# Optimization experiments

Measured on AMD Instinct MI355X. Metric: run time of the kernel, lower is better.

The kernel has to match this reference:

```python
import jax, jax.numpy as jnp
import numpy as np

E = 1024   # n_embd
H = 16     # n_heads
D = 64     # head_dim
G = 4      # n_kv_groups
F = 4096   # ffn hidden_dim
V = 32000  # vocab
L = 4      # n_layers (all full_attention)
B = 1
T = 2048
ROT = 16   # partial_rotary_factor 0.25 * head_dim 64, rounded to even
EPS = 1e-6
THETA = 10000.0


def rope_tables(seq_len):
    # matches compute_rope_params: inv_freq over even indices of rotary_dim
    inv_freq = 1.0 / (THETA ** (jnp.arange(0, ROT, 2, dtype=jnp.float32) / ROT))
    ang = jnp.arange(seq_len, dtype=jnp.float32)[:, None] * inv_freq[None, :]
    ang = jnp.concatenate([ang, ang], axis=1)  # [T, ROT]
    return jnp.cos(ang), jnp.sin(ang)


def rmsnorm(x, w):
    # torch RMSNorm: x * rsqrt(mean(x^2)+eps) * (1 + weight)
    xf = x.astype(jnp.float32)
    n = xf * jax.lax.rsqrt(jnp.mean(xf * xf, axis=-1, keepdims=True) + EPS)
    return (n * (1.0 + w)).astype(x.dtype)


def apply_rope(x, cos, sin):
    # x: [B, h, T, D]; cos/sin: [1, 1, T, ROT]; partial rotary on first ROT dims
    x_rot, x_pass = x[..., :ROT], x[..., ROT:]
    x1, x2 = x_rot[..., :ROT // 2], x_rot[..., ROT // 2:]
    rotated = jnp.concatenate([-x2, x1], axis=-1)
    return jnp.concatenate([x_rot * cos + rotated * sin, x_pass], axis=-1)


def _forward(tokens, emb, Wq, Wk, Wv, Wo, qn, kn, n1, n2, f1, f2, f3, fn, head):
    cos, sin = rope_tables(T)
    cos = cos[None, None]  # [1,1,T,ROT]
    sin = sin[None, None]
    mask = jnp.triu(jnp.ones((T, T), dtype=bool), k=1)  # True = masked
    scale = D ** -0.5
    x = emb[tokens]  # [B,T,E]

    def block(x, p):
        wq, wk, wv, wo, qw, kw, w1, w2, g1, g2, g3 = p
        h = rmsnorm(x, w1)
        # fused Q + gate projection -> [B,T,H,2D], chunk on last dim
        qg = (h @ wq).reshape(B, T, H, 2 * D)
        q = qg[..., :D].transpose(0, 2, 1, 3)            # [B,H,T,D]
        gate = qg[..., D:].reshape(B, T, H * D)          # [B,T,H*D]
        k = (h @ wk).reshape(B, T, G, D).transpose(0, 2, 1, 3)  # [B,G,T,D]
        v = (h @ wv).reshape(B, T, G, D).transpose(0, 2, 1, 3)
        q = rmsnorm(q, qw)
        k = rmsnorm(k, kw)
        q = apply_rope(q, cos, sin)
        k = apply_rope(k, cos, sin)
        k = jnp.repeat(k, H // G, axis=1)  # GQA expand -> [B,H,T,D]
        v = jnp.repeat(v, H // G, axis=1)
        scores = jnp.einsum('bhqd,bhkd->bhqk', q, k)
        scores = jnp.where(mask, -jnp.inf, scores) * scale
        w = jax.nn.softmax(scores.astype(jnp.float32), axis=-1).astype(q.dtype)
        ctx = jnp.einsum('bhqk,bhkd->bhqd', w, v)
        ctx = ctx.transpose(0, 2, 1, 3).reshape(B, T, H * D)
        ctx = ctx * jax.nn.sigmoid(gate)
        x = x + ctx @ wo
        h2 = rmsnorm(x, w2)
        ff = (jax.nn.silu(h2 @ g1) * (h2 @ g2)) @ g3
        return x + ff, None

    params = (Wq, Wk, Wv, Wo, qn, kn, n1, n2, f1, f2, f3)
    x, _ = jax.lax.scan(block, x, params)
    return rmsnorm(x, fn) @ head  # logits [B,T,V]


def setup_inputs() -> dict:
    key = jax.random.key(0)
    ks = jax.random.split(key, 16)
    s = 0.02
    rn = lambda k, shape, sc=s: jax.random.normal(k, shape, jnp.float32) * sc
    return {
        'tokens': jax.random.randint(ks[0], (B, T), 0, V),
        'emb': rn(ks[1], (V, E)),
        'Wq': rn(ks[2], (L, E, 2 * H * D)),
        'Wk': rn(ks[3], (L, E, G * D)),
        'Wv': rn(ks[4], (L, E, G * D)),
        'Wo': rn(ks[5], (L, H * D, E)),
        'qn': rn(ks[6], (L, D)),
        'kn': rn(ks[7], (L, D)),
        'n1': rn(ks[8], (L, E)),
        'n2': rn(ks[9], (L, E)),
        'f1': rn(ks[10], (L, E, F)),
        'f2': rn(ks[11], (L, E, F)),
        'f3': rn(ks[12], (L, F, E)),
        'fn': rn(ks[13], (E,)),
        'head': rn(ks[14], (E, V)),
    }


def reference(tokens, emb, Wq, Wk, Wv, Wo, qn, kn, n1, n2, f1, f2, f3, fn, head):
    return _forward(tokens, emb, Wq, Wk, Wv, Wo, qn, kn, n1, n2, f1, f2, f3, fn, head)
```

## Files before the change

kernel.cpp:

```cpp
#include <hip/hip_runtime.h>

#define T_LEN 2048
#define E_DIM 1024
#define H_N 16
#define G_N 4
#define D_H 64
#define F_DIM 4096
#define V_SZ 32000
#define L_N 4

typedef __attribute__((ext_vector_type(8))) __bf16 bf16x8;
typedef __attribute__((ext_vector_type(4))) float f32x4;

__device__ __forceinline__ unsigned short f2bf(float f){
  unsigned int u = __float_as_uint(f);
  unsigned int r = (u + 0x7FFFu + ((u >> 16) & 1u)) >> 16;
  return (unsigned short)r;
}

__device__ __forceinline__ f32x4 mfma16(bf16x8 a, bf16x8 b, f32x4 c){
  return __builtin_amdgcn_mfma_f32_16x16x32_bf16(a, b, c, 0, 0, 0);
}

__device__ __forceinline__ void gl16(const void* g, void* l){
  __builtin_amdgcn_global_load_lds((const __attribute__((address_space(1))) void*)g,
                                   (__attribute__((address_space(3))) void*)l, 16, 0, 0);
}

#define SBAR() __builtin_amdgcn_s_barrier()
#define LGK0() do{ asm volatile("s_waitcnt lgkmcnt(0)" ::: "memory"); __builtin_amdgcn_sched_barrier(0); }while(0)
#define VMC4() do{ asm volatile("s_waitcnt vmcnt(4)" ::: "memory"); __builtin_amdgcn_sched_barrier(0); }while(0)
#define VMC0() do{ asm volatile("s_waitcnt vmcnt(0)" ::: "memory"); __builtin_amdgcn_sched_barrier(0); }while(0)

#define QSCALE 0.1803368801111183f

__global__ __launch_bounds__(256) void embed_k(const float* __restrict__ emb,
                                               const int* __restrict__ tokens,
                                               float* __restrict__ x){
  int t = blockIdx.x;
  int tok = tokens[t];
  const float4* src = (const float4*)(emb + (size_t)tok * E_DIM);
  float4* dst = (float4*)(x + (size_t)t * E_DIM);
  dst[threadIdx.x] = src[threadIdx.x];
}

__global__ __launch_bounds__(256) void transpose_bf16(const float* __restrict__ src,
                                                      unsigned short* __restrict__ dst,
                                                      int R, int C){
  __shared__ float tile[32][33];
  int c0 = blockIdx.x * 32, r0 = blockIdx.y * 32;
  int tx = threadIdx.x & 31, ty = threadIdx.x >> 5;
  for (int i = 0; i < 4; i++){
    int r = ty + i * 8;
    tile[r][tx] = src[(size_t)(r0 + r) * C + c0 + tx];
  }
  __syncthreads();
  for (int i = 0; i < 4; i++){
    int r = ty + i * 8;
    dst[(size_t)(c0 + r) * R + r0 + tx] = f2bf(tile[tx][r]);
  }
}

__global__ __launch_bounds__(256) void rmsnorm_k(const float* __restrict__ x,
                                                 const float* __restrict__ w,
                                                 unsigned short* __restrict__ out){
  const int t = blockIdx.x, tid = threadIdx.x;
  const float4 v = ((const float4*)(x + (size_t)t * E_DIM))[tid];
  float ss = v.x*v.x + v.y*v.y + v.z*v.z + v.w*v.w;
  for (int m = 1; m < 64; m <<= 1) ss += __shfl_xor(ss, m);
  __shared__ float red[4];
  if ((tid & 63) == 0) red[tid >> 6] = ss;
  __syncthreads();
  ss = red[0] + red[1] + red[2] + red[3];
  const float r = rsqrtf(ss * (1.0f / E_DIM) + 1e-6f);
  const float4 wv = ((const float4*)w)[tid];
  ushort4 o;
  o.x = f2bf(v.x * r * (1.0f + wv.x));
  o.y = f2bf(v.y * r * (1.0f + wv.y));
  o.z = f2bf(v.z * r * (1.0f + wv.z));
  o.w = f2bf(v.w * r * (1.0f + wv.w));
  ((ushort4*)(out + (size_t)t * E_DIM))[tid] = o;
}

template<bool ADD>
__global__ __launch_bounds__(256) void gemm64_bt(const unsigned short* __restrict__ A,
                                                 const unsigned short* __restrict__ Bt,
                                                 float* __restrict__ C,
                                                 int M, int N, int K){
  __shared__ unsigned short As[64 * 32];
  __shared__ unsigned short Bs[128 * 32];
  const int tid = threadIdx.x;
  const int lane = tid & 63, w = tid >> 6;
  const int l15 = lane & 15, l4 = lane >> 4;

  const int chunk = gridDim.x >> 3;
  const int wgid = (blockIdx.x & 7) * chunk + (blockIdx.x >> 3);
  const int nm = M >> 6;
  const int bm = wgid % nm, bn = wgid / nm;
  const int m0 = bm * 64, n0 = bn * 128;

  const int r0 = tid >> 2;
  const int c0 = (tid & 3) << 3;

  const unsigned short* gA  = A  + (size_t)(m0 + r0) * K + c0;
  const unsigned short* gB0 = Bt + (size_t)(n0 + r0) * K + c0;
  const unsigned short* gB1 = Bt + (size_t)(n0 + 64 + r0) * K + c0;
  unsigned short* lA  = As + w * 512;
  unsigned short* lB0 = Bs + w * 512;
  unsigned short* lB1 = Bs + 2048 + w * 512;

  f32x4 acc[4][2] = {};

  for (int k0 = 0; k0 < K; k0 += 32){
    __syncthreads();
    gl16(gA  + k0, lA);
    gl16(gB0 + k0, lB0);
    gl16(gB1 + k0, lB1);
    __syncthreads();
    bf16x8 af[4], bfr[2];
    for (int i = 0; i < 4; i++)
      af[i] = *(const bf16x8*)&As[(i * 16 + l15) * 32 + l4 * 8];
    for (int j = 0; j < 2; j++)
      bfr[j] = *(const bf16x8*)&Bs[(w * 32 + j * 16 + l15) * 32 + l4 * 8];
    for (int i = 0; i < 4; i++)
      for (int j = 0; j < 2; j++)
        acc[i][j] = mfma16(af[i], bfr[j], acc[i][j]);
  }

  for (int i = 0; i < 4; i++)
    for (int j = 0; j < 2; j++){
      int col = n0 + w * 32 + j * 16 + l15;
      for (int r = 0; r < 4; r++){
        int row = m0 + i * 16 + l4 * 4 + r;
        size_t idx = (size_t)row * N + col;
        if (ADD) C[idx] += acc[i][j][r]; else C[idx] = acc[i][j][r];
      }
    }
}

__global__ __launch_bounds__(512, 2) void gemm256(const unsigned short* __restrict__ A,
                                                  const unsigned short* __restrict__ Bt,
                                                  float* __restrict__ C,
                                                  int M, int N, int K){
  __shared__ unsigned short lds[65536];
  const int tid = threadIdx.x;
  const int lane = tid & 63, w = tid >> 6;
  const int wm = w >> 2, wn = w & 3;
  const int l15 = lane & 15, l4 = lane >> 4;

  const int chunk = gridDim.x >> 3;
  const int wgid = ((int)blockIdx.x & 7) * chunk + ((int)blockIdx.x >> 3);
  const int nm = M >> 8;
  const int bm = wgid % nm, bn = wgid / nm;
  const int m0 = bm * 256, n0 = bn * 256;
  const int NT = K >> 6;

  const int srow = (lane >> 3);
  const int scol = lane & 7;

  auto stageA = [&](int b, int h, int kt){
    #pragma unroll
    for (int c = 0; c < 2; c++){
      int r = w * 16 + c * 8 + srow;
      const unsigned short* g = A + (size_t)(m0 + h * 128 + r) * K + kt * 64 + ((scol ^ (r & 7)) << 3);
      gl16(g, (char*)lds + (b * 2 + h) * 16384 + (w * 16 + c * 8) * 128);
    }
  };
  auto stageB = [&](int b, int h, int kt){
    #pragma unroll
    for (int c = 0; c < 2; c++){
      int r = w * 16 + c * 8 + srow;
      const unsigned short* g = Bt + (size_t)(n0 + h * 128 + r) * K + kt * 64 + ((scol ^ (r & 7)) << 3);
      gl16(g, (char*)lds + 65536 + (b * 2 + h) * 16384 + (w * 16 + c * 8) * 128);
    }
  };

  const int sl0 = ((l4)     ^ (l15 & 7)) << 4;
  const int sl1 = ((4 | l4) ^ (l15 & 7)) << 4;

  f32x4 acc[8][4] = {};
  bf16x8 aF[8], bF[8];

  stageA(0, 0, 0); stageA(0, 1, 0); stageB(0, 0, 0); stageB(0, 1, 0);
  if (NT > 1){ stageB(1, 0, 1); stageB(1, 1, 1); }
  VMC4();
  SBAR();

  for (int kt = 0; kt < NT; kt++){
    const int buf = kt & 1;
    const char* Ab = (const char*)lds + (buf * 2 + wm) * 16384;
    const char* Bb = (const char*)lds + 65536 + (buf * 2 + (wn >> 1)) * 16384;
    const int brbase = (wn & 1) * 64;

    #pragma unroll
    for (int mf = 0; mf < 4; mf++){
      int r = mf * 16 + l15;
      aF[mf * 2 + 0] = *(const bf16x8*)(Ab + r * 128 + sl0);
      aF[mf * 2 + 1] = *(const bf16x8*)(Ab + r * 128 + sl1);
    }
    #pragma unroll
    for (int nf = 0; nf < 2; nf++){
      int r = brbase + nf * 16 + l15;
      bF[nf * 2 + 0] = *(const bf16x8*)(Bb + r * 128 + sl0);
      bF[nf * 2 + 1] = *(const bf16x8*)(Bb + r * 128 + sl1);
    }
    if (kt + 1 < NT) stageA(buf ^ 1, 0, kt + 1);
    SBAR(); LGK0();
    __builtin_amdgcn_s_setprio(1);
    #pragma unroll
    for (int mf = 0; mf < 4; mf++)
      #pragma unroll
      for (int nf = 0; nf < 2; nf++){
        acc[mf][nf] = mfma16(aF[mf * 2 + 0], bF[nf * 2 + 0], acc[mf][nf]);
        acc[mf][nf] = mfma16(aF[mf * 2 + 1], bF[nf * 2 + 1], acc[mf][nf]);
      }
    __builtin_amdgcn_s_setprio(0);
    SBAR();

    #pragma unroll
    for (int nf = 2; nf < 4; nf++){
      int r = brbase + nf * 16 + l15;
      bF[nf * 2 + 0] = *(const bf16x8*)(Bb + r * 128 + sl0);
      bF[nf * 2 + 1] = *(const bf16x8*)(Bb + r * 128 + sl1);
    }
    if (kt + 1 < NT) stageA(buf ^ 1, 1, kt + 1);
    SBAR(); LGK0();
    __builtin_amdgcn_s_setprio(1);
    #pragma unroll
    for (int mf = 0; mf < 4; mf++)
      #pragma unroll
      for (int nf = 2; nf < 4; nf++){
        acc[mf][nf] = mfma16(aF[mf * 2 + 0], bF[nf * 2 + 0], acc[mf][nf]);
        acc[mf][nf] = mfma16(aF[mf * 2 + 1], bF[nf * 2 + 1], acc[mf][nf]);
      }
    __builtin_amdgcn_s_setprio(0);
    SBAR();

    #pragma unroll
    for (int mf = 0; mf < 4; mf++){
      int r = 64 + mf * 16 + l15;
      aF[mf * 2 + 0] = *(const bf16x8*)(Ab + r * 128 + sl0);
      aF[mf * 2 + 1] = *(const bf16x8*)(Ab + r * 128 + sl1);
    }
    if (kt + 2 < NT) stageB(buf, 0, kt + 2);
    SBAR(); LGK0();
    __builtin_amdgcn_s_setprio(1);
    #pragma unroll
    for (int mf = 0; mf < 4; mf++)
      #pragma unroll
      for (int nf = 2; nf < 4; nf++){
        acc[4 + mf][nf] = mfma16(aF[mf * 2 + 0], bF[nf * 2 + 0], acc[4 + mf][nf]);
        acc[4 + mf][nf] = mfma16(aF[mf * 2 + 1], bF[nf * 2 + 1], acc[4 + mf][nf]);
      }
    __builtin_amdgcn_s_setprio(0);
    SBAR();

    if (kt + 2 < NT) stageB(buf, 1, kt + 2);
    SBAR();
    __builtin_amdgcn_s_setprio(1);
    #pragma unroll
    for (int mf = 0; mf < 4; mf++)
      #pragma unroll
      for (int nf = 0; nf < 2; nf++){
        acc[4 + mf][nf] = mfma16(aF[mf * 2 + 0], bF[nf * 2 + 0], acc[4 + mf][nf]);
        acc[4 + mf][nf] = mfma16(aF[mf * 2 + 1], bF[nf * 2 + 1], acc[4 + mf][nf]);
      }
    __builtin_amdgcn_s_setprio(0);
    if (kt + 2 < NT) { VMC4(); } else { VMC0(); }
    SBAR();
  }

  #pragma unroll
  for (int mfg = 0; mfg < 8; mfg++){
    #pragma unroll
    for (int nf = 0; nf < 4; nf++){
      int col = n0 + wn * 64 + nf * 16 + l15;
      int row0 = m0 + wm * 128 + mfg * 16 + l4 * 4;
      #pragma unroll
      for (int r = 0; r < 4; r++)
        C[(size_t)(row0 + r) * N + col] = acc[mfg][nf][r];
    }
  }
}

__global__ __launch_bounds__(256) void qkvpost_k(const float* __restrict__ qkv,
                                                 const float* __restrict__ qn,
                                                 const float* __restrict__ kn,
                                                 unsigned short* __restrict__ qb,
                                                 unsigned short* __restrict__ kb,
                                                 unsigned short* __restrict__ vt){
  const int t = blockIdx.x;
  const int lane = threadIdx.x & 63, w = threadIdx.x >> 6;
  const int d = lane;
  const int fi = d & 7;
  const float invf = powf(10000.0f, -(float)fi * 0.125f);
  const float ang = (float)t * invf;
  const float c = cosf(ang), s = sinf(ang);

  for (int i = 0; i < 4; i++){
    int h = w * 4 + i;
    float v = qkv[(size_t)t * 2560 + h * 128 + d];
    float ss = v * v;
    for (int m = 1; m < 64; m <<= 1) ss += __shfl_xor(ss, m);
    float r = rsqrtf(ss * (1.0f / D_H) + 1e-6f);
    float xn = v * r * (1.0f + qn[d]);
    float partner = __shfl_xor(xn, 8);
    float o;
    if (d < 8)       o = xn * c - partner * s;
    else if (d < 16) o = xn * c + partner * s;
    else             o = xn;
    qb[((size_t)h * T_LEN + t) * D_H + d] = f2bf(o * QSCALE);
  }
  {
    float v = qkv[(size_t)t * 2560 + 2048 + w * 64 + d];
    float ss = v * v;
    for (int m = 1; m < 64; m <<= 1) ss += __shfl_xor(ss, m);
    float r = rsqrtf(ss * (1.0f / D_H) + 1e-6f);
    float xn = v * r * (1.0f + kn[d]);
    float partner = __shfl_xor(xn, 8);
    float o;
    if (d < 8)       o = xn * c - partner * s;
    else if (d < 16) o = xn * c + partner * s;
    else             o = xn;
    kb[((size_t)w * T_LEN + t) * D_H + d] = f2bf(o);
  }
  {
    float v = qkv[(size_t)t * 2560 + 2304 + w * 64 + d];
    vt[((size_t)(w * 64 + d)) * T_LEN + t] = f2bf(v);
  }
}

__global__ __launch_bounds__(64) void attn_k(const unsigned short* __restrict__ qb,
                                             const unsigned short* __restrict__ kb,
                                             const unsigned short* __restrict__ vt,
                                             const float* __restrict__ qkv,
                                             unsigned short* __restrict__ ctxg){
  const int qt = blockIdx.x, h = blockIdx.y;
  const int g = h >> 2;
  const int lane = threadIdx.x;
  const int l15 = lane & 15, l4 = lane >> 4;
  const int q0 = qt * 16;
  __shared__ unsigned short Pl[16][72];

  const bf16x8 aq0 = *(const bf16x8*)(qb + ((size_t)h * T_LEN + q0 + l15) * D_H + l4 * 8);
  const bf16x8 aq1 = *(const bf16x8*)(qb + ((size_t)h * T_LEN + q0 + l15) * D_H + 32 + l4 * 8);

  f32x4 acc[4] = {};
  float mrun[4], lpart[4];
  for (int j = 0; j < 4; j++){ mrun[j] = -1e30f; lpart[j] = 0.0f; }

  for (int kv0 = 0; kv0 <= q0 + 15; kv0 += 64){
    f32x4 sc[4];
    #pragma unroll
    for (int cp = 0; cp < 4; cp++){
      const unsigned short* kbase = kb + ((size_t)g * T_LEN + kv0 + cp * 16 + l15) * D_H + l4 * 8;
      bf16x8 bk0 = *(const bf16x8*)(kbase);
      bf16x8 bk1 = *(const bf16x8*)(kbase + 32);
      f32x4 z = {0.f, 0.f, 0.f, 0.f};
      z = mfma16(aq0, bk0, z);
      z = mfma16(aq1, bk1, z);
      sc[cp] = z;
    }
    float resc[4];
    #pragma unroll
    for (int j = 0; j < 4; j++){
      int r = q0 + l4 * 4 + j;
      #pragma unroll
      for (int cp = 0; cp < 4; cp++){
        int col = kv0 + cp * 16 + l15;
        sc[cp][j] = (col <= r) ? sc[cp][j] : -1e30f;
      }
      float mx = fmaxf(fmaxf(sc[0][j], sc[1][j]), fmaxf(sc[2][j], sc[3][j]));
      for (int off = 1; off < 16; off <<= 1) mx = fmaxf(mx, __shfl_xor(mx, off));
      float mnew = fmaxf(mrun[j], mx);
      resc[j] = exp2f(mrun[j] - mnew);
      mrun[j] = mnew;
      float ssum = 0.0f;
      #pragma unroll
      for (int cp = 0; cp < 4; cp++){
        float pv = exp2f(sc[cp][j] - mnew);
        sc[cp][j] = pv;
        ssum += pv;
      }
      lpart[j] = lpart[j] * resc[j] + ssum;
      #pragma unroll
      for (int nt = 0; nt < 4; nt++) acc[nt][j] *= resc[j];
    }
    __syncthreads();
    #pragma unroll
    for (int j = 0; j < 4; j++)
      #pragma unroll
      for (int cp = 0; cp < 4; cp++)
        Pl[l4 * 4 + j][cp * 16 + l15] = f2bf(sc[cp][j]);
    __syncthreads();
    const bf16x8 pa0 = *(const bf16x8*)&Pl[l15][l4 * 8];
    const bf16x8 pa1 = *(const bf16x8*)&Pl[l15][32 + l4 * 8];
    #pragma unroll
    for (int nt = 0; nt < 4; nt++){
      const unsigned short* vbase = vt + ((size_t)g * 64 + nt * 16 + l15) * T_LEN + kv0;
      bf16x8 bv0 = *(const bf16x8*)(vbase + l4 * 8);
      bf16x8 bv1 = *(const bf16x8*)(vbase + 32 + l4 * 8);
      acc[nt] = mfma16(pa1, bv1, mfma16(pa0, bv0, acc[nt]));
    }
  }

  #pragma unroll
  for (int j = 0; j < 4; j++)
    for (int off = 1; off < 16; off <<= 1) lpart[j] += __shfl_xor(lpart[j], off);

  #pragma unroll
  for (int j = 0; j < 4; j++){
    int r = q0 + l4 * 4 + j;
    float inv = 1.0f / lpart[j];
    #pragma unroll
    for (int nt = 0; nt < 4; nt++){
      int d = nt * 16 + l15;
      float gate = qkv[(size_t)r * 2560 + h * 128 + 64 + d];
      float val = acc[nt][j] * inv * (1.0f / (1.0f + __expf(-gate)));
      ctxg[(size_t)r * (H_N * D_H) + h * D_H + d] = f2bf(val);
    }
  }
}

__global__ __launch_bounds__(256) void silumul_k(const float* __restrict__ ff,
                                                 unsigned short* __restrict__ hg){
  size_t idx = ((size_t)blockIdx.x * 256 + threadIdx.x) * 4;
  size_t t = idx >> 12;
  size_t j = idx & 4095;
  const float4 u = *(const float4*)(ff + t * 8192 + j);
  const float4 gv = *(const float4*)(ff + t * 8192 + 4096 + j);
  ushort4 o;
  o.x = f2bf(u.x / (1.0f + __expf(-u.x)) * gv.x);
  o.y = f2bf(u.y / (1.0f + __expf(-u.y)) * gv.y);
  o.z = f2bf(u.z / (1.0f + __expf(-u.z)) * gv.z);
  o.w = f2bf(u.w / (1.0f + __expf(-u.w)) * gv.w);
  *(ushort4*)(hg + idx) = o;
}

extern "C" void kernel_launch(void* const* d_in, const int* in_sizes, int n_in,
                              void* d_out, int out_size, void* d_ws, size_t ws_size,
                              hipStream_t stream){
  (void)in_sizes; (void)n_in; (void)out_size; (void)ws_size;
  const int*   tokens = (const int*)d_in[0];
  const float* emb    = (const float*)d_in[1];
  const float* Wq     = (const float*)d_in[2];
  const float* Wk     = (const float*)d_in[3];
  const float* Wv     = (const float*)d_in[4];
  const float* Wo     = (const float*)d_in[5];
  const float* qn     = (const float*)d_in[6];
  const float* kn     = (const float*)d_in[7];
  const float* n1     = (const float*)d_in[8];
  const float* n2     = (const float*)d_in[9];
  const float* f1     = (const float*)d_in[10];
  const float* f2     = (const float*)d_in[11];
  const float* f3     = (const float*)d_in[12];
  const float* fn     = (const float*)d_in[13];
  const float* head   = (const float*)d_in[14];
  float* out = (float*)d_out;

  char* ws = (char*)d_ws;
  size_t off = 0;
  auto alloc = [&](size_t bytes)->char*{
    char* p = ws + off;
    off += (bytes + 255) & ~(size_t)255;
    return p;
  };
  float*          x       = (float*)alloc((size_t)T_LEN * E_DIM * 4);
  unsigned short* hbf     = (unsigned short*)alloc((size_t)T_LEN * E_DIM * 2);
  float*          qkvf    = (float*)alloc((size_t)T_LEN * 2560 * 4);
  unsigned short* qb      = (unsigned short*)alloc((size_t)H_N * T_LEN * D_H * 2);
  unsigned short* kb      = (unsigned short*)alloc((size_t)G_N * T_LEN * D_H * 2);
  unsigned short* vt      = (unsigned short*)alloc((size_t)G_N * D_H * T_LEN * 2);
  unsigned short* ctxg    = (unsigned short*)alloc((size_t)T_LEN * E_DIM * 2);
  float*          ff12    = (float*)alloc((size_t)T_LEN * 2 * F_DIM * 4);
  unsigned short* hg      = (unsigned short*)alloc((size_t)T_LEN * F_DIM * 2);
  unsigned short* wt_qkv  = (unsigned short*)alloc((size_t)2560 * E_DIM * 2);
  unsigned short* wt_o    = (unsigned short*)alloc((size_t)E_DIM * E_DIM * 2);
  unsigned short* wt_f12  = (unsigned short*)alloc((size_t)2 * F_DIM * E_DIM * 2);
  unsigned short* wt_f3   = (unsigned short*)alloc((size_t)E_DIM * F_DIM * 2);
  unsigned short* wt_head = (unsigned short*)alloc((size_t)V_SZ * E_DIM * 2);

  embed_k<<<T_LEN, 256, 0, stream>>>(emb, tokens, x);
  transpose_bf16<<<dim3(V_SZ / 32, E_DIM / 32), 256, 0, stream>>>(head, wt_head, E_DIM, V_SZ);

  for (int l = 0; l < L_N; l++){
    transpose_bf16<<<dim3(2048 / 32, 32), 256, 0, stream>>>(Wq + (size_t)l * E_DIM * 2048, wt_qkv, E_DIM, 2048);
    transpose_bf16<<<dim3(256 / 32, 32), 256, 0, stream>>>(Wk + (size_t)l * E_DIM * 256, wt_qkv + (size_t)2048 * E_DIM, E_DIM, 256);
    transpose_bf16<<<dim3(256 / 32, 32), 256, 0, stream>>>(Wv + (size_t)l * E_DIM * 256, wt_qkv + (size_t)2304 * E_DIM, E_DIM, 256);
    transpose_bf16<<<dim3(32, 32), 256, 0, stream>>>(Wo + (size_t)l * E_DIM * E_DIM, wt_o, E_DIM, E_DIM);
    transpose_bf16<<<dim3(F_DIM / 32, 32), 256, 0, stream>>>(f1 + (size_t)l * E_DIM * F_DIM, wt_f12, E_DIM, F_DIM);
    transpose_bf16<<<dim3(F_DIM / 32, 32), 256, 0, stream>>>(f2 + (size_t)l * E_DIM * F_DIM, wt_f12 + (size_t)F_DIM * E_DIM, E_DIM, F_DIM);
    transpose_bf16<<<dim3(E_DIM / 32, F_DIM / 32), 256, 0, stream>>>(f3 + (size_t)l * F_DIM * E_DIM, wt_f3, F_DIM, E_DIM);

    rmsnorm_k<<<T_LEN, 256, 0, stream>>>(x, n1 + l * E_DIM, hbf);
    gemm64_bt<false><<<(T_LEN / 64) * (2560 / 128), 256, 0, stream>>>(hbf, wt_qkv, qkvf, T_LEN, 2560, E_DIM);
    qkvpost_k<<<T_LEN, 256, 0, stream>>>(qkvf, qn + l * D_H, kn + l * D_H, qb, kb, vt);
    attn_k<<<dim3(T_LEN / 16, H_N), 64, 0, stream>>>(qb, kb, vt, qkvf, ctxg);
    gemm64_bt<true><<<(T_LEN / 64) * (E_DIM / 128), 256, 0, stream>>>(ctxg, wt_o, x, T_LEN, E_DIM, E_DIM);

    rmsnorm_k<<<T_LEN, 256, 0, stream>>>(x, n2 + l * E_DIM, hbf);
    gemm256<<<(T_LEN / 256) * (2 * F_DIM / 256), 512, 0, stream>>>(hbf, wt_f12, ff12, T_LEN, 2 * F_DIM, E_DIM);
    silumul_k<<<(T_LEN * F_DIM) / (256 * 4), 256, 0, stream>>>(ff12, hg);
    gemm64_bt<true><<<(T_LEN / 64) * (E_DIM / 128), 256, 0, stream>>>(hg, wt_f3, x, T_LEN, E_DIM, F_DIM);
  }

  rmsnorm_k<<<T_LEN, 256, 0, stream>>>(x, fn, hbf);
  gemm256<<<(T_LEN / 256) * (V_SZ / 256), 512, 0, stream>>>(hbf, wt_head, out, T_LEN, V_SZ, E_DIM);
}
```

Before: 1.676 ms.

## Fuse SiLU-gating into FFN up-projection GEMM epilogue with interleaved weights

Interleaves the f1 and f2 transposed weights in 16-column blocks so that each wave's adjacent MFMA fragments hold matching gate and up values. The gemm256 epilogue then computes silu(u)*g and writes bf16 directly, which removes the fp32 ff12 intermediate and the separate silumul kernel. The seven per-layer weight transpose launches are also merged into one prep_weights kernel to cut launch overhead. The cost is a templated epilogue and a weight layout that is tied to the fragment mapping.

```diff
diff --git a/kernel.cpp b/kernel.cpp
--- a/kernel.cpp
+++ b/kernel.cpp
@@ -58,6 +58,60 @@
   for (int i = 0; i < 4; i++){
     int r = ty + i * 8;
     dst[(size_t)(c0 + r) * R + r0 + tx] = f2bf(tile[tx][r]);
+  }
+}
+
+__device__ __forceinline__ void tr32(const float* __restrict__ src, unsigned short* __restrict__ dst,
+                                     int R, int C, int bx, int by, float* tile ){
+  int c0 = bx * 32, r0 = by * 32;
+  int tx = threadIdx.x & 31, ty = threadIdx.x >> 5;
+  for (int i = 0; i < 4; i++){
+    int r = ty + i * 8;
+    tile[r * 33 + tx] = src[(size_t)(r0 + r) * C + c0 + tx];
+  }
+  __syncthreads();
+  for (int i = 0; i < 4; i++){
+    int r = ty + i * 8;
+    dst[(size_t)(c0 + r) * R + r0 + tx] = f2bf(tile[tx * 33 + r]);
+  }
+}
+
+__global__ __launch_bounds__(256) void prep_weights(const float* __restrict__ Wq, const float* __restrict__ Wk,
+                                                    const float* __restrict__ Wv, const float* __restrict__ Wo,
+                                                    const float* __restrict__ f1, const float* __restrict__ f2,
+                                                    const float* __restrict__ f3,
+                                                    unsigned short* __restrict__ wt_qkv,
+                                                    unsigned short* __restrict__ wt_o,
+                                                    unsigned short* __restrict__ wt_f12i,
+                                                    unsigned short* __restrict__ wt_f3){
+  __shared__ float sh[1100];
+  int id = blockIdx.x;
+  if (id < 2048){ tr32(Wq, wt_qkv, 1024, 2048, id & 63, id >> 6, sh); return; }
+  id -= 2048;
+  if (id < 256){ tr32(Wk, wt_qkv + 2048 * 1024, 1024, 256, id & 7, id >> 3, sh); return; }
+  id -= 256;
+  if (id < 256){ tr32(Wv, wt_qkv + 2304 * 1024, 1024, 256, id & 7, id >> 3, sh); return; }
+  id -= 256;
+  if (id < 1024){ tr32(Wo, wt_o, 1024, 1024, id & 31, id >> 5, sh); return; }
+  id -= 1024;
+  if (id < 4096){ tr32(f3, wt_f3, 4096, 1024, id & 31, id >> 5, sh); return; }
+  id -= 4096;
+  {
+    int q = id & 255, kb = id >> 8;
+    float* t1 = sh; float* t2 = sh + 32 * 17;
+    int c = threadIdx.x & 15, kk0 = threadIdx.x >> 4;
+    for (int p = 0; p < 2; p++){
+      int kk = p * 16 + kk0;
+      t1[kk * 17 + c] = f1[(size_t)(kb * 32 + kk) * F_DIM + q * 16 + c];
+      t2[kk * 17 + c] = f2[(size_t)(kb * 32 + kk) * F_DIM + q * 16 + c];
+    }
+    __syncthreads();
+    int kk = threadIdx.x & 31, rb = threadIdx.x >> 5;
+    for (int i = 0; i < 4; i++){
+      int r = i * 8 + rb;
+      float v = (r < 16) ? t1[kk * 17 + r] : t2[kk * 17 + (r - 16)];
+      wt_f12i[(size_t)(q * 32 + r) * 1024 + kb * 32 + kk] = f2bf(v);
+    }
   }
 }
 
@@ -138,9 +192,11 @@
     }
 }
 
+template<int EPI>
 __global__ __launch_bounds__(512, 2) void gemm256(const unsigned short* __restrict__ A,
                                                   const unsigned short* __restrict__ Bt,
-                                                  float* __restrict__ C,
+                                                  float* __restrict__ outF,
+                                                  unsigned short* __restrict__ outH,
                                                   int M, int N, int K){
   __shared__ unsigned short lds[65536];
   const int tid = threadIdx.x;
@@ -270,15 +326,33 @@
     SBAR();
   }
 
-  #pragma unroll
-  for (int mfg = 0; mfg < 8; mfg++){
-    #pragma unroll
-    for (int nf = 0; nf < 4; nf++){
-      int col = n0 + wn * 64 + nf * 16 + l15;
-      int row0 = m0 + wm * 128 + mfg * 16 + l4 * 4;
-      #pragma unroll
-      for (int r = 0; r < 4; r++)
-        C[(size_t)(row0 + r) * N + col] = acc[mfg][nf][r];
+  if (EPI == 0){
+    #pragma unroll
+    for (int mfg = 0; mfg < 8; mfg++){
+      #pragma unroll
+      for (int nf = 0; nf < 4; nf++){
+        int col = n0 + wn * 64 + nf * 16 + l15;
+        int row0 = m0 + wm * 128 + mfg * 16 + l4 * 4;
+        #pragma unroll
+        for (int r = 0; r < 4; r++)
+          outF[(size_t)(row0 + r) * N + col] = acc[mfg][nf][r];
+      }
+    }
+  } else {
+    const int NH = N >> 1;
+    #pragma unroll
+    for (int mfg = 0; mfg < 8; mfg++){
+      #pragma unroll
+      for (int nfp = 0; nfp < 2; nfp++){
+        int col = (n0 >> 1) + wn * 32 + nfp * 16 + l15;
+        int row0 = m0 + wm * 128 + mfg * 16 + l4 * 4;
+        #pragma unroll
+        for (int r = 0; r < 4; r++){
+          float u = acc[mfg][nfp * 2 + 0][r];
+          float g = acc[mfg][nfp * 2 + 1][r];
+          outH[(size_t)(row0 + r) * NH + col] = f2bf(u / (1.0f + __expf(-u)) * g);
+        }
+      }
     }
   }
 }
@@ -420,21 +494,6 @@
       ctxg[(size_t)r * (H_N * D_H) + h * D_H + d] = f2bf(val);
     }
   }
-}
-
-__global__ __launch_bounds__(256) void silumul_k(const float* __restrict__ ff,
-                                                 unsigned short* __restrict__ hg){
-  size_t idx = ((size_t)blockIdx.x * 256 + threadIdx.x) * 4;
-  size_t t = idx >> 12;
-  size_t j = idx & 4095;
-  const float4 u = *(const float4*)(ff + t * 8192 + j);
-  const float4 gv = *(const float4*)(ff + t * 8192 + 4096 + j);
-  ushort4 o;
-  o.x = f2bf(u.x / (1.0f + __expf(-u.x)) * gv.x);
-  o.y = f2bf(u.y / (1.0f + __expf(-u.y)) * gv.y);
-  o.z = f2bf(u.z / (1.0f + __expf(-u.z)) * gv.z);
-  o.w = f2bf(u.w / (1.0f + __expf(-u.w)) * gv.w);
-  *(ushort4*)(hg + idx) = o;
 }
 
 extern "C" void kernel_launch(void* const* d_in, const int* in_sizes, int n_in,
@@ -472,11 +531,10 @@
   unsigned short* kb      = (unsigned short*)alloc((size_t)G_N * T_LEN * D_H * 2);
   unsigned short* vt      = (unsigned short*)alloc((size_t)G_N * D_H * T_LEN * 2);
   unsigned short* ctxg    = (unsigned short*)alloc((size_t)T_LEN * E_DIM * 2);
-  float*          ff12    = (float*)alloc((size_t)T_LEN * 2 * F_DIM * 4);
   unsigned short* hg      = (unsigned short*)alloc((size_t)T_LEN * F_DIM * 2);
   unsigned short* wt_qkv  = (unsigned short*)alloc((size_t)2560 * E_DIM * 2);
   unsigned short* wt_o    = (unsigned short*)alloc((size_t)E_DIM * E_DIM * 2);
-  unsigned short* wt_f12  = (unsigned short*)alloc((size_t)2 * F_DIM * E_DIM * 2);
+  unsigned short* wt_f12i = (unsigned short*)alloc((size_t)2 * F_DIM * E_DIM * 2);
   unsigned short* wt_f3   = (unsigned short*)alloc((size_t)E_DIM * F_DIM * 2);
   unsigned short* wt_head = (unsigned short*)alloc((size_t)V_SZ * E_DIM * 2);
 
@@ -484,13 +542,14 @@
   transpose_bf16<<<dim3(V_SZ / 32, E_DIM / 32), 256, 0, stream>>>(head, wt_head, E_DIM, V_SZ);
 
   for (int l = 0; l < L_N; l++){
-    transpose_bf16<<<dim3(2048 / 32, 32), 256, 0, stream>>>(Wq + (size_t)l * E_DIM * 2048, wt_qkv, E_DIM, 2048);
-    transpose_bf16<<<dim3(256 / 32, 32), 256, 0, stream>>>(Wk + (size_t)l * E_DIM * 256, wt_qkv + (size_t)2048 * E_DIM, E_DIM, 256);
-    transpose_bf16<<<dim3(256 / 32, 32), 256, 0, stream>>>(Wv + (size_t)l * E_DIM * 256, wt_qkv + (size_t)2304 * E_DIM, E_DIM, 256);
-    transpose_bf16<<<dim3(32, 32), 256, 0, stream>>>(Wo + (size_t)l * E_DIM * E_DIM, wt_o, E_DIM, E_DIM);
-    transpose_bf16<<<dim3(F_DIM / 32, 32), 256, 0, stream>>>(f1 + (size_t)l * E_DIM * F_DIM, wt_f12, E_DIM, F_DIM);
-    transpose_bf16<<<dim3(F_DIM / 32, 32), 256, 0, stream>>>(f2 + (size_t)l * E_DIM * F_DIM, wt_f12 + (size_t)F_DIM * E_DIM, E_DIM, F_DIM);
-    transpose_bf16<<<dim3(E_DIM / 32, F_DIM / 32), 256, 0, stream>>>(f3 + (size_t)l * F_DIM * E_DIM, wt_f3, F_DIM, E_DIM);
+    prep_weights<<<15872, 256, 0, stream>>>(Wq + (size_t)l * E_DIM * 2048,
+                                            Wk + (size_t)l * E_DIM * 256,
+                                            Wv + (size_t)l * E_DIM * 256,
+                                            Wo + (size_t)l * E_DIM * E_DIM,
+                                            f1 + (size_t)l * E_DIM * F_DIM,
+                                            f2 + (size_t)l * E_DIM * F_DIM,
+                                            f3 + (size_t)l * F_DIM * E_DIM,
+                                            wt_qkv, wt_o, wt_f12i, wt_f3);
 
     rmsnorm_k<<<T_LEN, 256, 0, stream>>>(x, n1 + l * E_DIM, hbf);
     gemm64_bt<false><<<(T_LEN / 64) * (2560 / 128), 256, 0, stream>>>(hbf, wt_qkv, qkvf, T_LEN, 2560, E_DIM);
@@ -499,11 +558,10 @@
     gemm64_bt<true><<<(T_LEN / 64) * (E_DIM / 128), 256, 0, stream>>>(ctxg, wt_o, x, T_LEN, E_DIM, E_DIM);
 
     rmsnorm_k<<<T_LEN, 256, 0, stream>>>(x, n2 + l * E_DIM, hbf);
-    gemm256<<<(T_LEN / 256) * (2 * F_DIM / 256), 512, 0, stream>>>(hbf, wt_f12, ff12, T_LEN, 2 * F_DIM, E_DIM);
-    silumul_k<<<(T_LEN * F_DIM) / (256 * 4), 256, 0, stream>>>(ff12, hg);
+    gemm256<1><<<(T_LEN / 256) * (2 * F_DIM / 256), 512, 0, stream>>>(hbf, wt_f12i, nullptr, hg, T_LEN, 2 * F_DIM, E_DIM);
     gemm64_bt<true><<<(T_LEN / 64) * (E_DIM / 128), 256, 0, stream>>>(hg, wt_f3, x, T_LEN, E_DIM, F_DIM);
   }
 
   rmsnorm_k<<<T_LEN, 256, 0, stream>>>(x, fn, hbf);
-  gemm256<<<(T_LEN / 256) * (V_SZ / 256), 512, 0, stream>>>(hbf, wt_head, out, T_LEN, V_SZ, E_DIM);
-}
+  gemm256<0><<<(T_LEN / 256) * (V_SZ / 256), 512, 0, stream>>>(hbf, wt_head, out, nullptr, T_LEN, V_SZ, E_DIM);
+}
```

Measured after the change: 1.569 ms. 6.4% less time.
